# Performance work log

Measured on AMD Instinct MI355X. Metric: run time of the kernel, lower is better.

## Reference

```python
import jax, jax.numpy as jnp
import numpy as np

H, E, K = 1024, 8, 2  # hidden_size, num_experts, top_k
B, S = 2, 4096


def setup_inputs() -> dict:
    key = jax.random.key(0)
    ks = jax.random.split(key, 5)
    s = 1.0 / np.sqrt(H)
    return {
        "x": jax.random.normal(ks[0], (B, S, H), dtype=jnp.float32),
        "ln_scale": jnp.ones((H,), jnp.float32),
        "ln_bias": jnp.zeros((H,), jnp.float32),
        "w1": (jax.random.normal(ks[1], (H, H), jnp.float32) * s),
        "b1": jnp.zeros((H,), jnp.float32),
        "w2": (jax.random.normal(ks[2], (H, E), jnp.float32) * s),
        "b2": jnp.zeros((E,), jnp.float32),
        "We": (jax.random.normal(ks[3], (E, H, H), jnp.float32) * s),
        "be": jnp.zeros((E, H), jnp.float32),
    }


def _layernorm(x, scale, bias, eps=1e-5):
    m = jnp.mean(x, axis=-1, keepdims=True)
    v = jnp.var(x, axis=-1, keepdims=True)
    return (x - m) * jax.lax.rsqrt(v + eps) * scale + bias


def reference(x, ln_scale, ln_bias, w1, b1, w2, b2, We, be):
    b, s, h = x.shape
    # --- router (BaseRouter): LN -> MLP -> softmax -> top-k -> renorm ---
    xn = _layernorm(x, ln_scale, ln_bias)
    hmid = jax.nn.relu(xn @ w1 + b1)
    logits = hmid @ w2 + b2                      # [B,S,E]
    probs = jax.nn.softmax(logits, axis=-1)
    topk_p, topk_i = jax.lax.top_k(probs, K)     # [B,S,K]
    topk_p = topk_p / jnp.sum(topk_p, axis=-1, keepdims=True)
    # sparse combine weights [B,S,E]: renormalized top-k gate, 0 elsewhere
    cw = jnp.sum(topk_p[..., None] * jax.nn.one_hot(topk_i, E, dtype=x.dtype), axis=-2)
    # --- expert dispatch / weighted combine ---
    t = b * s
    xf = x.reshape(t, h)
    cwf = cw.reshape(t, E)
    ye = jnp.einsum('th,ehd->etd', xf, We) + be[:, None, :]   # [E,T,H]
    out = jnp.einsum('te,etd->td', cwf, ye).reshape(b, s, h)
    # --- aux load-balance loss ---
    mean_p = jnp.mean(probs, axis=(0, 1))        # [E]
    aux = jnp.sum(mean_p * jnp.log(mean_p * E + 1e-9))
    return out, aux
```

## Files before the change

kernel.cpp:

```cpp
#include <hip/hip_runtime.h>
#include <hip/hip_fp16.h>

#define H 1024
#define E 8
#define TT 8192

typedef __attribute__((ext_vector_type(8))) short bf16x8;
typedef __attribute__((ext_vector_type(4))) float f32x4;

__device__ __forceinline__ unsigned short f2bf(float f) {
  unsigned int u = __float_as_uint(f);
  u += 0x7fffu + ((u >> 16) & 1u);
  return (unsigned short)(u >> 16);
}

__device__ __forceinline__ int swz(int row, int c) {
  return (row << 5) | (((c ^ (row >> 1)) & 3) << 3);
}

__global__ __launch_bounds__(64) void k_init(int* cnt, double* psum) {
  int t = threadIdx.x;
  if (t < E) { cnt[t] = 0; psum[t] = 0.0; }
}

__global__ __launch_bounds__(256) void k_cast_we(const float* __restrict__ we, unsigned short* __restrict__ wet) {
  __shared__ unsigned short tile[32][33];
  int e = blockIdx.z;
  int kb = blockIdx.x << 5, nb = blockIdx.y << 5;
  int t = threadIdx.x;
  int cc = t & 31, rr = t >> 5;
  size_t base = (size_t)e * H * H;
#pragma unroll
  for (int r = 0; r < 4; ++r) {
    int k = kb + rr + (r << 3);
    tile[rr + (r << 3)][cc] = f2bf(we[base + (size_t)k * H + nb + cc]);
  }
  __syncthreads();
#pragma unroll
  for (int r = 0; r < 4; ++r) {
    int n = nb + rr + (r << 3);
    wet[base + (size_t)n * H + kb + cc] = tile[cc][rr + (r << 3)];
  }
}

__global__ __launch_bounds__(256) void k_cast_w1(const float* __restrict__ w1, const float* __restrict__ lsc,
                                                 unsigned short* __restrict__ w1h, unsigned short* __restrict__ w1l) {
  __shared__ float tile[32][33];
  int kb = blockIdx.x << 5, nb = blockIdx.y << 5;
  int t = threadIdx.x;
  int cc = t & 31, rr = t >> 5;
#pragma unroll
  for (int r = 0; r < 4; ++r) {
    int k = kb + rr + (r << 3);
    tile[rr + (r << 3)][cc] = w1[(size_t)k * H + nb + cc] * lsc[k];
  }
  __syncthreads();
#pragma unroll
  for (int r = 0; r < 4; ++r) {
    int n = nb + rr + (r << 3);
    float v = tile[cc][rr + (r << 3)];
    unsigned short h = f2bf(v);
    float hv = __uint_as_float((unsigned)h << 16);
    unsigned short l = f2bf(v - hv);
    w1h[(size_t)n * H + kb + cc] = h;
    w1l[(size_t)n * H + kb + cc] = l;
  }
}

__global__ __launch_bounds__(256) void k_b1a(const float* __restrict__ w1, const float* __restrict__ lbi,
                                             float* __restrict__ part) {
  int bk = blockIdx.x, t = threadIdx.x;
  float a0 = 0, a1 = 0, a2 = 0, a3 = 0;
  for (int kk = 0; kk < 16; ++kk) {
    int k = (bk << 4) + kk;
    float lb = lbi[k];
    const float* row = &w1[(size_t)k * H];
    a0 = fmaf(lb, row[t], a0);
    a1 = fmaf(lb, row[t + 256], a1);
    a2 = fmaf(lb, row[t + 512], a2);
    a3 = fmaf(lb, row[t + 768], a3);
  }
  part[bk * H + t] = a0;
  part[bk * H + t + 256] = a1;
  part[bk * H + t + 512] = a2;
  part[bk * H + t + 768] = a3;
}

__global__ __launch_bounds__(256) void k_b1b(const float* __restrict__ part, const float* __restrict__ b1,
                                             float* __restrict__ b1eff) {
  int n = (blockIdx.x << 8) + threadIdx.x;
  float s = b1[n];
  for (int j = 0; j < 64; ++j) s += part[j * H + n];
  b1eff[n] = s;
}

__global__ __launch_bounds__(256) void k_stats(const float* __restrict__ x, float2* __restrict__ stats,
                                               unsigned short* __restrict__ xb) {
  int tok = blockIdx.x, t = threadIdx.x;
  const float4 v = *reinterpret_cast<const float4*>(&x[(size_t)tok * H + (t << 2)]);
  float s = v.x + v.y + v.z + v.w;
  float ss = v.x * v.x + v.y * v.y + v.z * v.z + v.w * v.w;
#pragma unroll
  for (int off = 32; off; off >>= 1) { s += __shfl_down(s, off); ss += __shfl_down(ss, off); }
  __shared__ float red[4][2];
  int lane = t & 63, wv = t >> 6;
  if (lane == 0) { red[wv][0] = s; red[wv][1] = ss; }
  __syncthreads();
  float fs = red[0][0] + red[1][0] + red[2][0] + red[3][0];
  float fss = red[0][1] + red[1][1] + red[2][1] + red[3][1];
  float mean = fs * (1.0f / H);
  float var = fss * (1.0f / H) - mean * mean;
  float rstd = rsqrtf(var + 1e-5f);
  if (t == 0) stats[tok] = make_float2(mean, rstd);
  ushort4 ob;
  ob.x = f2bf(v.x); ob.y = f2bf(v.y); ob.z = f2bf(v.z); ob.w = f2bf(v.w);
  *reinterpret_cast<ushort4*>(&xb[(size_t)tok * H + (t << 2)]) = ob;
}

__global__ __launch_bounds__(256) void k_router_mfma(
    const float* __restrict__ x, const float2* __restrict__ stats,
    const unsigned short* __restrict__ w1h, const unsigned short* __restrict__ w1l,
    const float* __restrict__ b1eff, const float* __restrict__ w2, float* __restrict__ plog) {
  __shared__ __align__(16) short Ah[4096], Al[4096], Bh[4096], Bl[4096];
  __shared__ float2 st[128];
  int t = threadIdx.x;
  int bm = blockIdx.x << 7, bn = blockIdx.y << 7;
  if (t < 128) st[t] = stats[bm + t];
  __syncthreads();
  int arow = t >> 1, ac0 = (t & 1) << 1;
  int brow = t >> 2, bc = t & 3;
  float2 mr = st[arow];
  float rs = mr.y, mb = -mr.x * mr.y;
  const float* xsrc = &x[(size_t)(bm + arow) * H + (ac0 << 3)];
  const unsigned short* s1 = &w1h[(size_t)(bn + brow) * H + (bc << 3)];
  const unsigned short* s2 = &w1h[(size_t)(bn + brow + 64) * H + (bc << 3)];
  const unsigned short* s3 = &w1l[(size_t)(bn + brow) * H + (bc << 3)];
  const unsigned short* s4 = &w1l[(size_t)(bn + brow + 64) * H + (bc << 3)];
  float4 va0 = *(const float4*)(xsrc + 0), va1 = *(const float4*)(xsrc + 4);
  float4 va2 = *(const float4*)(xsrc + 8), va3 = *(const float4*)(xsrc + 12);
  int4 vb0 = *(const int4*)s1, vb1 = *(const int4*)s2, vb2 = *(const int4*)s3, vb3 = *(const int4*)s4;
  int lane = t & 63, wv = t >> 6;
  int wr = (wv >> 1) << 6, wc = (wv & 1) << 6;
  int l15 = lane & 15, lgp = lane >> 4;
  f32x4 acc[4][4];
#pragma unroll
  for (int i = 0; i < 4; ++i)
#pragma unroll
    for (int j = 0; j < 4; ++j) acc[i][j] = f32x4{0.f, 0.f, 0.f, 0.f};
  for (int kt = 0; kt < 32; ++kt) {
    float zz[16];
    zz[0] = fmaf(va0.x, rs, mb); zz[1] = fmaf(va0.y, rs, mb);
    zz[2] = fmaf(va0.z, rs, mb); zz[3] = fmaf(va0.w, rs, mb);
    zz[4] = fmaf(va1.x, rs, mb); zz[5] = fmaf(va1.y, rs, mb);
    zz[6] = fmaf(va1.z, rs, mb); zz[7] = fmaf(va1.w, rs, mb);
    zz[8] = fmaf(va2.x, rs, mb); zz[9] = fmaf(va2.y, rs, mb);
    zz[10] = fmaf(va2.z, rs, mb); zz[11] = fmaf(va2.w, rs, mb);
    zz[12] = fmaf(va3.x, rs, mb); zz[13] = fmaf(va3.y, rs, mb);
    zz[14] = fmaf(va3.z, rs, mb); zz[15] = fmaf(va3.w, rs, mb);
    unsigned hw[8], lw[8];
#pragma unroll
    for (int p = 0; p < 8; ++p) {
      unsigned ua = __float_as_uint(zz[2 * p]), ub = __float_as_uint(zz[2 * p + 1]);
      hw[p] = (ua >> 16) | (ub & 0xffff0000u);
      float la = zz[2 * p] - __uint_as_float(ua & 0xffff0000u);
      float lb = zz[2 * p + 1] - __uint_as_float(ub & 0xffff0000u);
      lw[p] = (__float_as_uint(la) >> 16) | (__float_as_uint(lb) & 0xffff0000u);
    }
    __syncthreads();
    *(int4*)&Ah[swz(arow, ac0)] = make_int4(hw[0], hw[1], hw[2], hw[3]);
    *(int4*)&Ah[swz(arow, ac0 + 1)] = make_int4(hw[4], hw[5], hw[6], hw[7]);
    *(int4*)&Al[swz(arow, ac0)] = make_int4(lw[0], lw[1], lw[2], lw[3]);
    *(int4*)&Al[swz(arow, ac0 + 1)] = make_int4(lw[4], lw[5], lw[6], lw[7]);
    *(int4*)&Bh[swz(brow, bc)] = vb0;
    *(int4*)&Bh[swz(brow + 64, bc)] = vb1;
    *(int4*)&Bl[swz(brow, bc)] = vb2;
    *(int4*)&Bl[swz(brow + 64, bc)] = vb3;
    __syncthreads();
    if (kt + 1 < 32) {
      xsrc += 32; s1 += 32; s2 += 32; s3 += 32; s4 += 32;
      va0 = *(const float4*)(xsrc + 0); va1 = *(const float4*)(xsrc + 4);
      va2 = *(const float4*)(xsrc + 8); va3 = *(const float4*)(xsrc + 12);
      vb0 = *(const int4*)s1; vb1 = *(const int4*)s2; vb2 = *(const int4*)s3; vb3 = *(const int4*)s4;
    }
    bf16x8 bh[4], bl[4];
#pragma unroll
    for (int j = 0; j < 4; ++j) {
      bh[j] = *(const bf16x8*)&Bh[swz(wc + (j << 4) + l15, lgp)];
      bl[j] = *(const bf16x8*)&Bl[swz(wc + (j << 4) + l15, lgp)];
    }
#pragma unroll
    for (int i = 0; i < 4; ++i) {
      bf16x8 ah = *(const bf16x8*)&Ah[swz(wr + (i << 4) + l15, lgp)];
      bf16x8 al = *(const bf16x8*)&Al[swz(wr + (i << 4) + l15, lgp)];
#pragma unroll
      for (int j = 0; j < 4; ++j) {
        acc[i][j] = __builtin_amdgcn_mfma_f32_16x16x32_bf16(ah, bh[j], acc[i][j], 0, 0, 0);
        acc[i][j] = __builtin_amdgcn_mfma_f32_16x16x32_bf16(ah, bl[j], acc[i][j], 0, 0, 0);
        acc[i][j] = __builtin_amdgcn_mfma_f32_16x16x32_bf16(al, bh[j], acc[i][j], 0, 0, 0);
      }
    }
  }
  float w2r[4][8], b1r[4];
#pragma unroll
  for (int j = 0; j < 4; ++j) {
    int col = bn + wc + (j << 4) + l15;
    float4 p0 = *(const float4*)&w2[(size_t)col * E];
    float4 p1 = *(const float4*)&w2[(size_t)col * E + 4];
    w2r[j][0] = p0.x; w2r[j][1] = p0.y; w2r[j][2] = p0.z; w2r[j][3] = p0.w;
    w2r[j][4] = p1.x; w2r[j][5] = p1.y; w2r[j][6] = p1.z; w2r[j][7] = p1.w;
    b1r[j] = b1eff[col];
  }
#pragma unroll
  for (int i = 0; i < 4; ++i)
#pragma unroll
    for (int j = 0; j < 4; ++j)
#pragma unroll
      for (int r = 0; r < 4; ++r) acc[i][j][r] = fmaxf(acc[i][j][r] + b1r[j], 0.f);
  int wh = wc >> 6;
  size_t pbase = ((size_t)(blockIdx.y * 2 + wh) * TT + bm) * E;
#pragma unroll
  for (int e = 0; e < E; ++e) {
    float se[4][4];
#pragma unroll
    for (int i = 0; i < 4; ++i)
#pragma unroll
      for (int r = 0; r < 4; ++r)
        se[i][r] = acc[i][0][r] * w2r[0][e] + acc[i][1][r] * w2r[1][e] +
                   acc[i][2][r] * w2r[2][e] + acc[i][3][r] * w2r[3][e];
#pragma unroll
    for (int off = 1; off < 16; off <<= 1)
#pragma unroll
      for (int i = 0; i < 4; ++i)
#pragma unroll
        for (int r = 0; r < 4; ++r) se[i][r] += __shfl_xor(se[i][r], off);
    if (l15 == 0) {
#pragma unroll
      for (int i = 0; i < 4; ++i)
#pragma unroll
        for (int r = 0; r < 4; ++r) {
          int row = wr + (i << 4) + (lgp << 2) + r;
          plog[pbase + (size_t)row * E + e] = se[i][r];
        }
    }
  }
}

__global__ __launch_bounds__(256) void k_top(const float* __restrict__ plog, const float* __restrict__ b2,
                                             int* __restrict__ topE, float* __restrict__ topW,
                                             int* __restrict__ listIdx, float* __restrict__ listW,
                                             int* __restrict__ cnt, double* __restrict__ psum) {
  int t = threadIdx.x, lane = t & 63;
  int tok = (blockIdx.x << 8) + t;
  float lg[E], p[E];
  float4 ba = *reinterpret_cast<const float4*>(b2);
  float4 bb = *reinterpret_cast<const float4*>(b2 + 4);
  lg[0] = ba.x; lg[1] = ba.y; lg[2] = ba.z; lg[3] = ba.w;
  lg[4] = bb.x; lg[5] = bb.y; lg[6] = bb.z; lg[7] = bb.w;
#pragma unroll
  for (int nb = 0; nb < 16; ++nb) {
    const float* pp = &plog[((size_t)nb * TT + tok) * E];
    float4 q0 = *reinterpret_cast<const float4*>(pp);
    float4 q1 = *reinterpret_cast<const float4*>(pp + 4);
    lg[0] += q0.x; lg[1] += q0.y; lg[2] += q0.z; lg[3] += q0.w;
    lg[4] += q1.x; lg[5] += q1.y; lg[6] += q1.z; lg[7] += q1.w;
  }
  float m = lg[0];
#pragma unroll
  for (int e = 1; e < E; ++e) m = fmaxf(m, lg[e]);
  float s = 0.f;
#pragma unroll
  for (int e = 0; e < E; ++e) { p[e] = __expf(lg[e] - m); s += p[e]; }
  float inv = 1.f / s;
#pragma unroll
  for (int e = 0; e < E; ++e) p[e] *= inv;
  {
    float ps[E];
#pragma unroll
    for (int e = 0; e < E; ++e) ps[e] = p[e];
#pragma unroll
    for (int off = 1; off < 64; off <<= 1)
#pragma unroll
      for (int e = 0; e < E; ++e) ps[e] += __shfl_xor(ps[e], off);
    if (lane == 0)
#pragma unroll
      for (int e = 0; e < E; ++e) atomicAdd(&psum[e], (double)ps[e]);
  }
  int e0 = 0;
#pragma unroll
  for (int e = 1; e < E; ++e) if (p[e] > p[e0]) e0 = e;
  int e1 = (e0 == 0) ? 1 : 0;
#pragma unroll
  for (int e = 0; e < E; ++e) if (e != e0 && p[e] > p[e1]) e1 = e;
  float rsw = 1.f / (p[e0] + p[e1]);
  float w0 = p[e0] * rsw, w1v = p[e1] * rsw;
  topE[tok << 1] = e0; topE[(tok << 1) + 1] = e1;
  topW[tok << 1] = w0; topW[(tok << 1) + 1] = w1v;
  unsigned long long lt = (1ull << lane) - 1ull;
#pragma unroll
  for (int e = 0; e < E; ++e) {
    unsigned long long m0 = __ballot(e0 == e);
    unsigned long long m1 = __ballot(e1 == e);
    int n0 = __popcll(m0), total = n0 + __popcll(m1);
    if (total == 0) continue;
    int leader = __ffsll(m0 | m1) - 1;
    int base = 0;
    if (lane == leader) base = atomicAdd(&cnt[e], total);
    base = __shfl(base, leader);
    if (e0 == e) {
      int pos = e * TT + base + __popcll(m0 & lt);
      listIdx[pos] = (tok << 1); listW[pos] = w0;
    }
    if (e1 == e) {
      int pos = e * TT + base + n0 + __popcll(m1 & lt);
      listIdx[pos] = (tok << 1) | 1; listW[pos] = w1v;
    }
  }
}

__global__ __launch_bounds__(256) void k_expert_gemm(const unsigned short* __restrict__ xb,
                                                     const unsigned short* __restrict__ wet,
                                                     const int* __restrict__ listIdx, const float* __restrict__ listW,
                                                     const int* __restrict__ cnt, unsigned short* __restrict__ ys) {
  int e = blockIdx.z;
  int c = cnt[e];
  int r0 = blockIdx.x << 7;
  if (r0 >= c) return;
  int n0 = blockIdx.y << 7;
  __shared__ __align__(16) short A[4096], B[4096];
  __shared__ int gi[128];
  __shared__ float gw[128];
  int t = threadIdx.x;
  if (t < 128) {
    int rr = r0 + t;
    gi[t] = (rr < c) ? listIdx[e * TT + rr] : -1;
    gw[t] = (rr < c) ? listW[e * TT + rr] : 0.f;
  }
  __syncthreads();
  int brow = t >> 2, bc = t & 3;
  int pk1 = gi[brow], pk2 = gi[brow + 64];
  int tokA1 = (pk1 < 0) ? 0 : (pk1 >> 1);
  int tokA2 = (pk2 < 0) ? 0 : (pk2 >> 1);
  const unsigned short* a1 = &xb[(size_t)tokA1 * H + (bc << 3)];
  const unsigned short* a2 = &xb[(size_t)tokA2 * H + (bc << 3)];
  size_t wbase = (size_t)e * H * H;
  const unsigned short* b1 = &wet[wbase + (size_t)(n0 + brow) * H + (bc << 3)];
  const unsigned short* b2 = &wet[wbase + (size_t)(n0 + brow + 64) * H + (bc << 3)];
  int4 va0 = *(const int4*)a1, va1 = *(const int4*)a2;
  int4 vb0 = *(const int4*)b1, vb1 = *(const int4*)b2;
  int lane = t & 63, wv = t >> 6;
  int wr = (wv >> 1) << 6, wc = (wv & 1) << 6;
  int l15 = lane & 15, lgp = lane >> 4;
  f32x4 acc[4][4];
#pragma unroll
  for (int i = 0; i < 4; ++i)
#pragma unroll
    for (int j = 0; j < 4; ++j) acc[i][j] = f32x4{0.f, 0.f, 0.f, 0.f};
  for (int kt = 0; kt < 32; ++kt) {
    __syncthreads();
    *(int4*)&A[swz(brow, bc)] = va0;
    *(int4*)&A[swz(brow + 64, bc)] = va1;
    *(int4*)&B[swz(brow, bc)] = vb0;
    *(int4*)&B[swz(brow + 64, bc)] = vb1;
    __syncthreads();
    if (kt + 1 < 32) {
      a1 += 32; a2 += 32; b1 += 32; b2 += 32;
      va0 = *(const int4*)a1; va1 = *(const int4*)a2;
      vb0 = *(const int4*)b1; vb1 = *(const int4*)b2;
    }
    bf16x8 bq[4];
#pragma unroll
    for (int j = 0; j < 4; ++j) bq[j] = *(const bf16x8*)&B[swz(wc + (j << 4) + l15, lgp)];
#pragma unroll
    for (int i = 0; i < 4; ++i) {
      bf16x8 af = *(const bf16x8*)&A[swz(wr + (i << 4) + l15, lgp)];
#pragma unroll
      for (int j = 0; j < 4; ++j)
        acc[i][j] = __builtin_amdgcn_mfma_f32_16x16x32_bf16(af, bq[j], acc[i][j], 0, 0, 0);
    }
  }
#pragma unroll
  for (int i = 0; i < 4; ++i) {
#pragma unroll
    for (int r = 0; r < 4; ++r) {
      int row = wr + (i << 4) + (lgp << 2) + r;
      int pk = gi[row];
      if (pk < 0) continue;
      int tok = pk >> 1, slot = pk & 1;
      float w = gw[row];
      size_t ob = ((size_t)slot * TT + tok) * H + n0 + wc + l15;
#pragma unroll
      for (int j = 0; j < 4; ++j) ys[ob + (j << 4)] = __half_as_ushort(__float2half(w * acc[i][j][r]));
    }
  }
}

__global__ __launch_bounds__(256) void k_combine(const unsigned short* __restrict__ ys, const int* __restrict__ topE,
                                                 const float* __restrict__ topW, const float* __restrict__ be,
                                                 float* __restrict__ out) {
  int tok = blockIdx.x, t = threadIdx.x;
  int e0 = topE[tok << 1], e1 = topE[(tok << 1) + 1];
  float w0 = topW[tok << 1], w1v = topW[(tok << 1) + 1];
  int h = t << 2;
  size_t base = (size_t)tok * H + h;
  ushort4 a = *reinterpret_cast<const ushort4*>(&ys[base]);
  ushort4 b = *reinterpret_cast<const ushort4*>(&ys[(size_t)TT * H + base]);
  float4 b0 = *reinterpret_cast<const float4*>(&be[e0 * H + h]);
  float4 b1v = *reinterpret_cast<const float4*>(&be[e1 * H + h]);
  float4 o;
  o.x = __half2float(__ushort_as_half(a.x)) + __half2float(__ushort_as_half(b.x)) + w0 * b0.x + w1v * b1v.x;
  o.y = __half2float(__ushort_as_half(a.y)) + __half2float(__ushort_as_half(b.y)) + w0 * b0.y + w1v * b1v.y;
  o.z = __half2float(__ushort_as_half(a.z)) + __half2float(__ushort_as_half(b.z)) + w0 * b0.z + w1v * b1v.z;
  o.w = __half2float(__ushort_as_half(a.w)) + __half2float(__ushort_as_half(b.w)) + w0 * b0.w + w1v * b1v.w;
  *reinterpret_cast<float4*>(&out[base]) = o;
}

__global__ __launch_bounds__(64) void k_aux(const double* __restrict__ psum, float* __restrict__ outAux) {
  if (threadIdx.x == 0) {
    double a = 0.0;
    for (int e = 0; e < E; ++e) {
      double mp = psum[e] / (double)TT;
      a += mp * log(mp * (double)E + 1e-9);
    }
    outAux[0] = (float)a;
  }
}

extern "C" void kernel_launch(void* const* d_in, const int* in_sizes, int n_in, void* d_out, int out_size, void* d_ws,
                              size_t ws_size, hipStream_t stream) {
  const float* x = (const float*)d_in[0];
  const float* lsc = (const float*)d_in[1];
  const float* lbi = (const float*)d_in[2];
  const float* w1 = (const float*)d_in[3];
  const float* b1 = (const float*)d_in[4];
  const float* w2 = (const float*)d_in[5];
  const float* b2 = (const float*)d_in[6];
  const float* we = (const float*)d_in[7];
  const float* be = (const float*)d_in[8];
  float* out = (float*)d_out;
  char* ws = (char*)d_ws;

  char* p = ws;
  float2* stats = (float2*)p; p += TT * 8;
  int* topE = (int*)p; p += TT * 2 * 4;
  float* topW = (float*)p; p += TT * 2 * 4;
  int* listIdx = (int*)p; p += E * TT * 4;
  float* listW = (float*)p; p += E * TT * 4;
  int* cnt = (int*)p; p += 256;
  double* psum = (double*)p; p += 2048;
  float* b1eff = (float*)p; p += H * 4;
  float* part = (float*)p; p += 64 * H * 4;
  unsigned short* xb = (unsigned short*)(ws + (2u << 20));
  unsigned short* wet = (unsigned short*)(ws + (18u << 20));
  unsigned short* w1h = (unsigned short*)(ws + (34u << 20));
  unsigned short* w1l = (unsigned short*)(ws + (36u << 20));
  float* plog = (float*)(ws + (38u << 20));
  unsigned short* ys = (unsigned short*)(ws + (34u << 20));

  k_init<<<1, 64, 0, stream>>>(cnt, psum);
  k_cast_w1<<<dim3(32, 32), 256, 0, stream>>>(w1, lsc, w1h, w1l);
  k_b1a<<<64, 256, 0, stream>>>(w1, lbi, part);
  k_b1b<<<4, 256, 0, stream>>>(part, b1, b1eff);
  k_cast_we<<<dim3(32, 32, E), 256, 0, stream>>>(we, wet);
  k_stats<<<TT, 256, 0, stream>>>(x, stats, xb);
  k_router_mfma<<<dim3(TT / 128, H / 128), 256, 0, stream>>>(x, stats, w1h, w1l, b1eff, w2, plog);
  k_top<<<TT / 256, 256, 0, stream>>>(plog, b2, topE, topW, listIdx, listW, cnt, psum);
  k_expert_gemm<<<dim3(TT / 128, H / 128, E), 256, 0, stream>>>(xb, wet, listIdx, listW, cnt, ys);
  k_combine<<<TT, 256, 0, stream>>>(ys, topE, topW, be, out);
  k_aux<<<1, 64, 0, stream>>>(psum, out + (size_t)TT * H);
}
```

Measured before the change: 227.5 us.

## Double-buffer router and expert GEMM tiles with direct global-to-LDS loads

Both the router GEMM and the expert GEMM now use two LDS buffers and fetch the next K-tile with global_load_lds (direct global-to-LDS DMA) while MFMAs run on the current tile. This cuts the per-iteration barriers from two to one and removes the register staging round-trip for the B tiles (and the gathered A tiles in the expert GEMM). In exchange, LDS use doubles, which may lower occupancy. Correctness now depends on the precomputed swizzled destination offsets matching the layout the MFMA reads expect.

```diff
diff --git a/kernel.cpp b/kernel.cpp
--- a/kernel.cpp
+++ b/kernel.cpp
@@ -16,6 +16,11 @@
 
 __device__ __forceinline__ int swz(int row, int c) {
   return (row << 5) | (((c ^ (row >> 1)) & 3) << 3);
+}
+
+__device__ __forceinline__ void gld16(void* lds, const void* g) {
+  __builtin_amdgcn_global_load_lds((const __attribute__((address_space(1))) void*)g,
+                                   (__attribute__((address_space(3))) void*)lds, 16, 0, 0);
 }
 
 __global__ __launch_bounds__(64) void k_init(int* cnt, double* psum) {
@@ -121,42 +126,46 @@
     const float* __restrict__ x, const float2* __restrict__ stats,
     const unsigned short* __restrict__ w1h, const unsigned short* __restrict__ w1l,
     const float* __restrict__ b1eff, const float* __restrict__ w2, float* __restrict__ plog) {
-  __shared__ __align__(16) short Ah[4096], Al[4096], Bh[4096], Bl[4096];
-  __shared__ float2 st[128];
+  __shared__ __align__(16) short At[2][8192];
+  __shared__ __align__(16) short Bt[2][8192];
   int t = threadIdx.x;
   int bm = blockIdx.x << 7, bn = blockIdx.y << 7;
-  if (t < 128) st[t] = stats[bm + t];
-  __syncthreads();
+  int w = t >> 6, lane = t & 63;
+  int s0 = (w << 8) + lane;
+  int r0_ = s0 >> 2, cg0 = (s0 & 3) ^ ((r0_ >> 1) & 3);
+  int s1 = s0 + 64, r1_ = s1 >> 2, cg1 = (s1 & 3) ^ ((r1_ >> 1) & 3);
+  int s2 = s0 + 128, r2_ = s2 >> 2, cg2 = (s2 & 3) ^ ((r2_ >> 1) & 3);
+  int s3 = s0 + 192, r3_ = s3 >> 2, cg3 = (s3 & 3) ^ ((r3_ >> 1) & 3);
+  const unsigned short* srcB0 =
+      ((r0_ < 128) ? &w1h[(size_t)(bn + r0_) * H] : &w1l[(size_t)(bn + r0_ - 128) * H]) + (cg0 << 3);
+  const unsigned short* srcB1 =
+      ((r1_ < 128) ? &w1h[(size_t)(bn + r1_) * H] : &w1l[(size_t)(bn + r1_ - 128) * H]) + (cg1 << 3);
+  const unsigned short* srcB2 =
+      ((r2_ < 128) ? &w1h[(size_t)(bn + r2_) * H] : &w1l[(size_t)(bn + r2_ - 128) * H]) + (cg2 << 3);
+  const unsigned short* srcB3 =
+      ((r3_ < 128) ? &w1h[(size_t)(bn + r3_) * H] : &w1l[(size_t)(bn + r3_ - 128) * H]) + (cg3 << 3);
+  int dB0 = (w << 11), dB1 = dB0 + 512, dB2 = dB0 + 1024, dB3 = dB0 + 1536;
   int arow = t >> 1, ac0 = (t & 1) << 1;
-  int brow = t >> 2, bc = t & 3;
-  float2 mr = st[arow];
-  float rs = mr.y, mb = -mr.x * mr.y;
+  float2 mr = stats[bm + arow];
+  float rsc = mr.y, mb = -mr.x * mr.y;
   const float* xsrc = &x[(size_t)(bm + arow) * H + (ac0 << 3)];
-  const unsigned short* s1 = &w1h[(size_t)(bn + brow) * H + (bc << 3)];
-  const unsigned short* s2 = &w1h[(size_t)(bn + brow + 64) * H + (bc << 3)];
-  const unsigned short* s3 = &w1l[(size_t)(bn + brow) * H + (bc << 3)];
-  const unsigned short* s4 = &w1l[(size_t)(bn + brow + 64) * H + (bc << 3)];
-  float4 va0 = *(const float4*)(xsrc + 0), va1 = *(const float4*)(xsrc + 4);
-  float4 va2 = *(const float4*)(xsrc + 8), va3 = *(const float4*)(xsrc + 12);
-  int4 vb0 = *(const int4*)s1, vb1 = *(const int4*)s2, vb2 = *(const int4*)s3, vb3 = *(const int4*)s4;
-  int lane = t & 63, wv = t >> 6;
-  int wr = (wv >> 1) << 6, wc = (wv & 1) << 6;
-  int l15 = lane & 15, lgp = lane >> 4;
-  f32x4 acc[4][4];
-#pragma unroll
-  for (int i = 0; i < 4; ++i)
-#pragma unroll
-    for (int j = 0; j < 4; ++j) acc[i][j] = f32x4{0.f, 0.f, 0.f, 0.f};
-  for (int kt = 0; kt < 32; ++kt) {
+  int wA0 = swz(arow, ac0), wA1 = swz(arow, ac0 + 1);
+  int wL0 = swz(arow + 128, ac0), wL1 = swz(arow + 128, ac0 + 1);
+  float4 va0, va1, va2, va3;
+  auto ldx = [&]() {
+    va0 = *(const float4*)(xsrc + 0); va1 = *(const float4*)(xsrc + 4);
+    va2 = *(const float4*)(xsrc + 8); va3 = *(const float4*)(xsrc + 12);
+  };
+  auto split_store = [&](int b) {
     float zz[16];
-    zz[0] = fmaf(va0.x, rs, mb); zz[1] = fmaf(va0.y, rs, mb);
-    zz[2] = fmaf(va0.z, rs, mb); zz[3] = fmaf(va0.w, rs, mb);
-    zz[4] = fmaf(va1.x, rs, mb); zz[5] = fmaf(va1.y, rs, mb);
-    zz[6] = fmaf(va1.z, rs, mb); zz[7] = fmaf(va1.w, rs, mb);
-    zz[8] = fmaf(va2.x, rs, mb); zz[9] = fmaf(va2.y, rs, mb);
-    zz[10] = fmaf(va2.z, rs, mb); zz[11] = fmaf(va2.w, rs, mb);
-    zz[12] = fmaf(va3.x, rs, mb); zz[13] = fmaf(va3.y, rs, mb);
-    zz[14] = fmaf(va3.z, rs, mb); zz[15] = fmaf(va3.w, rs, mb);
+    zz[0] = fmaf(va0.x, rsc, mb); zz[1] = fmaf(va0.y, rsc, mb);
+    zz[2] = fmaf(va0.z, rsc, mb); zz[3] = fmaf(va0.w, rsc, mb);
+    zz[4] = fmaf(va1.x, rsc, mb); zz[5] = fmaf(va1.y, rsc, mb);
+    zz[6] = fmaf(va1.z, rsc, mb); zz[7] = fmaf(va1.w, rsc, mb);
+    zz[8] = fmaf(va2.x, rsc, mb); zz[9] = fmaf(va2.y, rsc, mb);
+    zz[10] = fmaf(va2.z, rsc, mb); zz[11] = fmaf(va2.w, rsc, mb);
+    zz[12] = fmaf(va3.x, rsc, mb); zz[13] = fmaf(va3.y, rsc, mb);
+    zz[14] = fmaf(va3.z, rsc, mb); zz[15] = fmaf(va3.w, rsc, mb);
     unsigned hw[8], lw[8];
 #pragma unroll
     for (int p = 0; p < 8; ++p) {
@@ -166,32 +175,43 @@
       float lb = zz[2 * p + 1] - __uint_as_float(ub & 0xffff0000u);
       lw[p] = (__float_as_uint(la) >> 16) | (__float_as_uint(lb) & 0xffff0000u);
     }
-    __syncthreads();
-    *(int4*)&Ah[swz(arow, ac0)] = make_int4(hw[0], hw[1], hw[2], hw[3]);
-    *(int4*)&Ah[swz(arow, ac0 + 1)] = make_int4(hw[4], hw[5], hw[6], hw[7]);
-    *(int4*)&Al[swz(arow, ac0)] = make_int4(lw[0], lw[1], lw[2], lw[3]);
-    *(int4*)&Al[swz(arow, ac0 + 1)] = make_int4(lw[4], lw[5], lw[6], lw[7]);
-    *(int4*)&Bh[swz(brow, bc)] = vb0;
-    *(int4*)&Bh[swz(brow + 64, bc)] = vb1;
-    *(int4*)&Bl[swz(brow, bc)] = vb2;
-    *(int4*)&Bl[swz(brow + 64, bc)] = vb3;
-    __syncthreads();
-    if (kt + 1 < 32) {
-      xsrc += 32; s1 += 32; s2 += 32; s3 += 32; s4 += 32;
-      va0 = *(const float4*)(xsrc + 0); va1 = *(const float4*)(xsrc + 4);
-      va2 = *(const float4*)(xsrc + 8); va3 = *(const float4*)(xsrc + 12);
-      vb0 = *(const int4*)s1; vb1 = *(const int4*)s2; vb2 = *(const int4*)s3; vb3 = *(const int4*)s4;
+    *(int4*)&At[b][wA0] = make_int4(hw[0], hw[1], hw[2], hw[3]);
+    *(int4*)&At[b][wA1] = make_int4(hw[4], hw[5], hw[6], hw[7]);
+    *(int4*)&At[b][wL0] = make_int4(lw[0], lw[1], lw[2], lw[3]);
+    *(int4*)&At[b][wL1] = make_int4(lw[4], lw[5], lw[6], lw[7]);
+  };
+  int wr = (w >> 1) << 6, wc = (w & 1) << 6;
+  int l15 = lane & 15, lgp = lane >> 4;
+  f32x4 acc[4][4];
+#pragma unroll
+  for (int i = 0; i < 4; ++i)
+#pragma unroll
+    for (int j = 0; j < 4; ++j) acc[i][j] = f32x4{0.f, 0.f, 0.f, 0.f};
+  ldx();
+  gld16(&Bt[0][dB0], srcB0); gld16(&Bt[0][dB1], srcB1);
+  gld16(&Bt[0][dB2], srcB2); gld16(&Bt[0][dB3], srcB3);
+  split_store(0);
+  asm volatile("s_waitcnt vmcnt(0) lgkmcnt(0)" ::: "memory");
+  __builtin_amdgcn_s_barrier();
+  for (int kt = 0; kt < 32; ++kt) {
+    int b = kt & 1;
+    if (kt < 31) {
+      xsrc += 32;
+      ldx();
+      srcB0 += 32; srcB1 += 32; srcB2 += 32; srcB3 += 32;
+      gld16(&Bt[b ^ 1][dB0], srcB0); gld16(&Bt[b ^ 1][dB1], srcB1);
+      gld16(&Bt[b ^ 1][dB2], srcB2); gld16(&Bt[b ^ 1][dB3], srcB3);
     }
     bf16x8 bh[4], bl[4];
 #pragma unroll
     for (int j = 0; j < 4; ++j) {
-      bh[j] = *(const bf16x8*)&Bh[swz(wc + (j << 4) + l15, lgp)];
-      bl[j] = *(const bf16x8*)&Bl[swz(wc + (j << 4) + l15, lgp)];
+      bh[j] = *(const bf16x8*)&Bt[b][swz(wc + (j << 4) + l15, lgp)];
+      bl[j] = *(const bf16x8*)&Bt[b][swz(128 + wc + (j << 4) + l15, lgp)];
     }
 #pragma unroll
     for (int i = 0; i < 4; ++i) {
-      bf16x8 ah = *(const bf16x8*)&Ah[swz(wr + (i << 4) + l15, lgp)];
-      bf16x8 al = *(const bf16x8*)&Al[swz(wr + (i << 4) + l15, lgp)];
+      bf16x8 ah = *(const bf16x8*)&At[b][swz(wr + (i << 4) + l15, lgp)];
+      bf16x8 al = *(const bf16x8*)&At[b][swz(128 + wr + (i << 4) + l15, lgp)];
 #pragma unroll
       for (int j = 0; j < 4; ++j) {
         acc[i][j] = __builtin_amdgcn_mfma_f32_16x16x32_bf16(ah, bh[j], acc[i][j], 0, 0, 0);
@@ -199,6 +219,9 @@
         acc[i][j] = __builtin_amdgcn_mfma_f32_16x16x32_bf16(al, bh[j], acc[i][j], 0, 0, 0);
       }
     }
+    if (kt < 31) split_store(b ^ 1);
+    asm volatile("s_waitcnt vmcnt(0) lgkmcnt(0)" ::: "memory");
+    __builtin_amdgcn_s_barrier();
   }
   float w2r[4][8], b1r[4];
 #pragma unroll
@@ -326,7 +349,7 @@
   int r0 = blockIdx.x << 7;
   if (r0 >= c) return;
   int n0 = blockIdx.y << 7;
-  __shared__ __align__(16) short A[4096], B[4096];
+  __shared__ __align__(16) short A[2][4096], B[2][4096];
   __shared__ int gi[128];
   __shared__ float gw[128];
   int t = threadIdx.x;
@@ -336,47 +359,47 @@
     gw[t] = (rr < c) ? listW[e * TT + rr] : 0.f;
   }
   __syncthreads();
-  int brow = t >> 2, bc = t & 3;
-  int pk1 = gi[brow], pk2 = gi[brow + 64];
-  int tokA1 = (pk1 < 0) ? 0 : (pk1 >> 1);
-  int tokA2 = (pk2 < 0) ? 0 : (pk2 >> 1);
-  const unsigned short* a1 = &xb[(size_t)tokA1 * H + (bc << 3)];
-  const unsigned short* a2 = &xb[(size_t)tokA2 * H + (bc << 3)];
+  int w = t >> 6, lane = t & 63;
+  int s0 = (w << 7) + lane, s1 = s0 + 64;
+  int rA0 = s0 >> 2, cg0 = (s0 & 3) ^ ((rA0 >> 1) & 3);
+  int rA1 = s1 >> 2, cg1 = (s1 & 3) ^ ((rA1 >> 1) & 3);
+  int pk0 = gi[rA0], pk1 = gi[rA1];
+  const unsigned short* srcA0 = &xb[(size_t)((pk0 < 0) ? 0 : (pk0 >> 1)) * H + (cg0 << 3)];
+  const unsigned short* srcA1 = &xb[(size_t)((pk1 < 0) ? 0 : (pk1 >> 1)) * H + (cg1 << 3)];
   size_t wbase = (size_t)e * H * H;
-  const unsigned short* b1 = &wet[wbase + (size_t)(n0 + brow) * H + (bc << 3)];
-  const unsigned short* b2 = &wet[wbase + (size_t)(n0 + brow + 64) * H + (bc << 3)];
-  int4 va0 = *(const int4*)a1, va1 = *(const int4*)a2;
-  int4 vb0 = *(const int4*)b1, vb1 = *(const int4*)b2;
-  int lane = t & 63, wv = t >> 6;
-  int wr = (wv >> 1) << 6, wc = (wv & 1) << 6;
+  const unsigned short* srcB0 = &wet[wbase + (size_t)(n0 + rA0) * H + (cg0 << 3)];
+  const unsigned short* srcB1 = &wet[wbase + (size_t)(n0 + rA1) * H + (cg1 << 3)];
+  int d0 = (w << 10), d1 = d0 + 512;
+  int wr = (w >> 1) << 6, wc = (w & 1) << 6;
   int l15 = lane & 15, lgp = lane >> 4;
   f32x4 acc[4][4];
 #pragma unroll
   for (int i = 0; i < 4; ++i)
 #pragma unroll
     for (int j = 0; j < 4; ++j) acc[i][j] = f32x4{0.f, 0.f, 0.f, 0.f};
+  gld16(&A[0][d0], srcA0); gld16(&A[0][d1], srcA1);
+  gld16(&B[0][d0], srcB0); gld16(&B[0][d1], srcB1);
+  asm volatile("s_waitcnt vmcnt(0)" ::: "memory");
+  __builtin_amdgcn_s_barrier();
   for (int kt = 0; kt < 32; ++kt) {
-    __syncthreads();
-    *(int4*)&A[swz(brow, bc)] = va0;
-    *(int4*)&A[swz(brow + 64, bc)] = va1;
-    *(int4*)&B[swz(brow, bc)] = vb0;
-    *(int4*)&B[swz(brow + 64, bc)] = vb1;
-    __syncthreads();
-    if (kt + 1 < 32) {
-      a1 += 32; a2 += 32; b1 += 32; b2 += 32;
-      va0 = *(const int4*)a1; va1 = *(const int4*)a2;
-      vb0 = *(const int4*)b1; vb1 = *(const int4*)b2;
+    int b = kt & 1;
+    if (kt < 31) {
+      srcA0 += 32; srcA1 += 32; srcB0 += 32; srcB1 += 32;
+      gld16(&A[b ^ 1][d0], srcA0); gld16(&A[b ^ 1][d1], srcA1);
+      gld16(&B[b ^ 1][d0], srcB0); gld16(&B[b ^ 1][d1], srcB1);
     }
     bf16x8 bq[4];
 #pragma unroll
-    for (int j = 0; j < 4; ++j) bq[j] = *(const bf16x8*)&B[swz(wc + (j << 4) + l15, lgp)];
+    for (int j = 0; j < 4; ++j) bq[j] = *(const bf16x8*)&B[b][swz(wc + (j << 4) + l15, lgp)];
 #pragma unroll
     for (int i = 0; i < 4; ++i) {
-      bf16x8 af = *(const bf16x8*)&A[swz(wr + (i << 4) + l15, lgp)];
+      bf16x8 af = *(const bf16x8*)&A[b][swz(wr + (i << 4) + l15, lgp)];
 #pragma unroll
       for (int j = 0; j < 4; ++j)
         acc[i][j] = __builtin_amdgcn_mfma_f32_16x16x32_bf16(af, bq[j], acc[i][j], 0, 0, 0);
     }
+    asm volatile("s_waitcnt vmcnt(0) lgkmcnt(0)" ::: "memory");
+    __builtin_amdgcn_s_barrier();
   }
 #pragma unroll
   for (int i = 0; i < 4; ++i) {
@@ -386,10 +409,10 @@
       int pk = gi[row];
       if (pk < 0) continue;
       int tok = pk >> 1, slot = pk & 1;
-      float w = gw[row];
+      float wgt = gw[row];
       size_t ob = ((size_t)slot * TT + tok) * H + n0 + wc + l15;
 #pragma unroll
-      for (int j = 0; j < 4; ++j) ys[ob + (j << 4)] = __half_as_ushort(__float2half(w * acc[i][j][r]));
+      for (int j = 0; j < 4; ++j) ys[ob + (j << 4)] = __half_as_ushort(__float2half(wgt * acc[i][j][r]));
     }
   }
 }
```

Measured after the change: 241.0 us. +5.9%, slower.
